# Performance work log

Hardware: AMD Instinct MI355X
Metric: run time of the kernel (lower is better)

## Reference

```python
import jax, jax.numpy as jnp
import numpy as np

SOFTCAP = 50.0
EPS = 1e-6
N_HEADS, D_HEAD = 16, 64


def _rms(x, w):
    return x * jax.lax.rsqrt(jnp.mean(x * x, axis=-1, keepdims=True) + EPS) * w


def _rope(x, cos, sin):
    # Faithful to source: apply_rope uses x.size(1) as the position axis, but is
    # called on (B, H, T, Dh) tensors, so positions are indexed by HEAD index.
    n = x.shape[1]
    x1, x2 = x[..., 0::2], x[..., 1::2]
    c = cos[:n][None, :, None, :]
    s = sin[:n][None, :, None, :]
    return jnp.stack([x1 * c - x2 * s, x1 * s + x2 * c], axis=-1).reshape(x.shape)


def setup_inputs() -> dict:
    key = jax.random.key(0)
    ks = jax.random.split(key, 12)
    L, D, H, Dh, Dff, V, B, T = 6, 1024, N_HEADS, D_HEAD, 4096, 32000, 1, 1024
    r = lambda k, shape: jax.random.normal(k, shape, dtype=jnp.float32) * 0.02
    return {
        'x': jax.random.randint(ks[0], (B, T), 0, V, dtype=jnp.int32),
        'embed': r(ks[1], (V, D)),
        'ln1': jnp.ones((L, D), jnp.float32),
        'Wq': r(ks[2], (L, H * Dh, D)),
        'Wk': r(ks[3], (L, H * Dh, D)),
        'Wv': r(ks[4], (L, H * Dh, D)),
        'Wo': r(ks[5], (L, D, H * Dh)),
        'qn': jnp.ones((L, Dh), jnp.float32),
        'kn': jnp.ones((L, Dh), jnp.float32),
        'ln2': jnp.ones((L, D), jnp.float32),
        'Wg': r(ks[6], (L, Dff, D)),
        'Wu': r(ks[7], (L, Dff, D)),
        'Wd': r(ks[8], (L, D, Dff)),
        'ln_out': jnp.ones((D,), jnp.float32),
    }


def reference(x, embed, ln1, Wq, Wk, Wv, Wo, qn, kn, ln2, Wg, Wu, Wd, ln_out):
    B, T = x.shape
    H, Dh = N_HEADS, D_HEAD
    scale = Dh ** -0.5
    # RoPE tables (theta=10000)
    freqs = 1.0 / (10000.0 ** (jnp.arange(0, Dh, 2, dtype=jnp.float32) / Dh))
    ang = jnp.arange(T, dtype=jnp.float32)[:, None] * freqs[None, :]
    cos, sin = jnp.cos(ang), jnp.sin(ang)
    mask = jnp.triu(jnp.ones((T, T), dtype=bool), k=1)  # True above diagonal

    h = embed[x]  # (B, T, D)

    def block(h, p):
        l1, wq, wk, wv, wo, qnw, knw, l2, wg, wu, wd = p
        hn = _rms(h, l1)
        q = (hn @ wq.T).reshape(B, T, H, Dh).transpose(0, 2, 1, 3)  # (B,H,T,Dh)
        k = (hn @ wk.T).reshape(B, T, H, Dh).transpose(0, 2, 1, 3)
        v = (hn @ wv.T).reshape(B, T, H, Dh).transpose(0, 2, 1, 3)
        q = _rope(_rms(q, qnw), cos, sin)
        k = _rope(_rms(k, knw), cos, sin)
        scores = jnp.einsum('bhtd,bhsd->bhts', q, k) * scale
        scores = SOFTCAP * jnp.tanh(scores / SOFTCAP)
        scores = jnp.where(mask[None, None], -jnp.inf, scores)
        attn = jax.nn.softmax(scores, axis=-1)
        o = jnp.einsum('bhts,bhsd->bhtd', attn, v)
        o = o.transpose(0, 2, 1, 3).reshape(B, T, H * Dh)
        h = h + o @ wo.T
        hn2 = _rms(h, l2)
        h = h + (jax.nn.silu(hn2 @ wg.T) * (hn2 @ wu.T)) @ wd.T
        return h, None

    h, _ = jax.lax.scan(block, h, (ln1, Wq, Wk, Wv, Wo, qn, kn, ln2, Wg, Wu, Wd))
    # tied embed/head
    logits = _rms(h, ln_out) @ embed.T  # (B, T, V)
    return logits
```

## Files before the change

### kernel.cpp

```cpp
#include <hip/hip_runtime.h>
#include <math.h>
#include <type_traits>

typedef __bf16 bf16_t;
typedef bf16_t bf16x4 __attribute__((ext_vector_type(4)));
typedef bf16_t bf16x8 __attribute__((ext_vector_type(8)));
typedef float  f32x4  __attribute__((ext_vector_type(4)));

#define RMS_EPS 1e-6f

enum { EP_STORE = 0, EP_RESID = 1, EP_SPLIT = 2, EP_SILU = 3, EP_QKV = 4 };

static __device__ __forceinline__ f32x4 mfma16(bf16x8 a, bf16x8 b, f32x4 c) {
    return __builtin_amdgcn_mfma_f32_16x16x32_bf16(a, b, c, 0, 0, 0);
}

#define GLDS(gp, lp) __builtin_amdgcn_global_load_lds( \
    (const __attribute__((address_space(1))) void*)(gp), \
    (__attribute__((address_space(3))) void*)(lp), 16, 0, 0)

template<int N> static __device__ __forceinline__ void vmwait() {
    if constexpr (N == 0)      asm volatile("s_waitcnt vmcnt(0)" ::: "memory");
    else if constexpr (N == 2) asm volatile("s_waitcnt vmcnt(2)" ::: "memory");
    else if constexpr (N == 3) asm volatile("s_waitcnt vmcnt(3)" ::: "memory");
    else if constexpr (N == 4) asm volatile("s_waitcnt vmcnt(4)" ::: "memory");
    else if constexpr (N == 6) asm volatile("s_waitcnt vmcnt(6)" ::: "memory");
    else if constexpr (N == 8) asm volatile("s_waitcnt vmcnt(8)" ::: "memory");
    __builtin_amdgcn_sched_barrier(0);
}
static __device__ __forceinline__ void bar() { __builtin_amdgcn_s_barrier(); }

template<int BM, int BN, int WR, int WC, int PLANES, int EPIL, int MINW, int DEPTH>
__global__ __launch_bounds__(WR * WC * 64, MINW)
void gemm_bf16(const bf16_t* __restrict__ Ah, const bf16_t* __restrict__ Al,
               const bf16_t* __restrict__ Bh,
               float* __restrict__ Cf, bf16_t* __restrict__ Ch, bf16_t* __restrict__ Cl,
               int K, int lda, int ldb, int ldc, long long sC,
               const float* __restrict__ qnw, const float* __restrict__ knw)
{
    constexpr int ASZ = BM * 32, BSZ = BN * 32;
    constexpr int NW = WR * WC;
    constexpr int NLD = (BM / 16 * (PLANES >= 2 ? 2 : 1) + BN / 16) / NW;
    __shared__ __align__(16) bf16_t sAh[DEPTH][ASZ], sBh[DEPTH][BSZ];
    __shared__ __align__(16) bf16_t sAl[PLANES >= 2 ? DEPTH : 1][PLANES >= 2 ? ASZ : 8];

    const int gx = gridDim.x;
    int id = blockIdx.x + gx * blockIdx.y;
    if (gridDim.z == 1) {
        int nwg = gx * gridDim.y;
        int q = nwg >> 3, r = nwg & 7;
        int xcd = id & 7, ix = id >> 3;
        id = (xcd < r ? xcd * (q + 1) : r * (q + 1) + (xcd - r) * q) + ix;
    }
    const int bm = id % gx, bn = id / gx;
    const int row0 = bm * BM, col0 = bn * BN;

    const size_t kofs = (size_t)blockIdx.z * K;
    Ah += kofs;  Bh += kofs;
    if constexpr (PLANES >= 2) Al += kofs;

    const int tid = threadIdx.x, lane = tid & 63, wave = tid >> 6;
    const int lr = lane & 15, lg = lane >> 4;
    constexpr int WM = BM / WR, WN = BN / WC, MF = WM / 16, NF = WN / 16;
    const int wr = wave / WC, wc = wave % WC;

    f32x4 acc[MF][NF];
    #pragma unroll
    for (int m = 0; m < MF; ++m)
        #pragma unroll
        for (int n = 0; n < NF; ++n) acc[m][n] = (f32x4){0.f, 0.f, 0.f, 0.f};

    auto stage = [&](int k0, int p) {
        #pragma unroll
        for (int i = wave; i < BM / 16; i += NW) {
            int s = i * 64 + lane, rr = s >> 2, c = s & 3;
            size_t go = (size_t)(row0 + rr) * lda + k0 + ((c ^ ((rr >> 1) & 3)) << 3);
            GLDS(Ah + go, &sAh[p][i * 512]);
            if constexpr (PLANES >= 2) GLDS(Al + go, &sAl[p][i * 512]);
        }
        #pragma unroll
        for (int i = wave; i < BN / 16; i += NW) {
            int s = i * 64 + lane, rr = s >> 2, c = s & 3;
            size_t go = (size_t)(col0 + rr) * ldb + k0 + ((c ^ ((rr >> 1) & 3)) << 3);
            GLDS(Bh + go, &sBh[p][i * 512]);
        }
    };

    auto compute = [&](int p) {
        bf16x8 ahf[MF], alf[MF], bhf[NF];
        #pragma unroll
        for (int m = 0; m < MF; ++m) {
            int rr = wr * WM + m * 16 + lr;
            int by = rr * 64 + ((lg ^ ((rr >> 1) & 3)) << 4);
            ahf[m] = *(const bf16x8*)((const char*)&sAh[p][0] + by);
            if constexpr (PLANES >= 2)
                alf[m] = *(const bf16x8*)((const char*)&sAl[p][0] + by);
        }
        #pragma unroll
        for (int n = 0; n < NF; ++n) {
            int rr = wc * WN + n * 16 + lr;
            int by = rr * 64 + ((lg ^ ((rr >> 1) & 3)) << 4);
            bhf[n] = *(const bf16x8*)((const char*)&sBh[p][0] + by);
        }
        #pragma unroll
        for (int m = 0; m < MF; ++m)
            #pragma unroll
            for (int n = 0; n < NF; ++n) {
                acc[m][n] = mfma16(ahf[m], bhf[n], acc[m][n]);
                if constexpr (PLANES >= 2)
                    acc[m][n] = mfma16(alf[m], bhf[n], acc[m][n]);
            }
    };

    if constexpr (DEPTH == 3) {
        const int NC = K >> 5;
        stage(0, 0);
        stage(32, 1);
        for (int j = 0; j + 2 < NC; ++j) {
            stage(32 * (j + 2), (j + 2) % 3);
            vmwait<2 * NLD>(); bar();
            compute(j % 3);
            bar();
        }
        vmwait<NLD>(); bar();
        compute((K >> 5) >= 2 ? ((K >> 5) - 2) % 3 : 0);
        vmwait<0>(); bar();
        compute(((K >> 5) - 1) % 3);
    } else {
        stage(0, 0);
        int k0 = 32;
        for (; k0 + 32 < K; k0 += 64) {
            stage(k0, 1);
            vmwait<NLD>(); bar();
            compute(0);
            bar();
            stage(k0 + 32, 0);
            vmwait<NLD>(); bar();
            compute(1);
            bar();
        }
        stage(k0, 1);
        vmwait<NLD>(); bar();
        compute(0);
        bar();
        vmwait<0>(); bar();
        compute(1);
    }

    if constexpr (EPIL == EP_QKV) {
        const int colbase = col0 + wc * WN;
        const int typ = colbase >> 10;
        const float* nw = (typ == 0) ? qnw : knw;
        const int hh = (colbase - typ * 1024) >> 6;
        constexpr float kLogF = -0.41524101186092029f;
        #pragma unroll
        for (int m = 0; m < MF; ++m)
            #pragma unroll
            for (int r = 0; r < 4; ++r) {
                int grow = row0 + wr * WM + m * 16 + lg * 4 + r;
                if (typ < 2) {
                    float ss = 0.f;
                    #pragma unroll
                    for (int n = 0; n < NF; ++n) {
                        float v = acc[m][n][r];
                        ss += v * v;
                    }
                    ss += __shfl_xor(ss, 1, 64);
                    ss += __shfl_xor(ss, 2, 64);
                    ss += __shfl_xor(ss, 4, 64);
                    ss += __shfl_xor(ss, 8, 64);
                    float inv = rsqrtf(ss * (1.0f / 64.0f) + RMS_EPS);
                    #pragma unroll
                    for (int n = 0; n < NF; ++n) {
                        int i = n * 16 + lr;
                        float x = acc[m][n][r] * inv * nw[i];
                        float p = __shfl_xor(x, 1, 64);
                        float f = exp2f((float)(i >> 1) * kLogF);
                        float ang = (float)hh * f;
                        float cs = cosf(ang), sn = sinf(ang);
                        float o = (lr & 1) ? (p * sn + x * cs) : (x * cs - p * sn);
                        Ch[(size_t)grow * ldc + colbase + i] = (bf16_t)o;
                    }
                } else {
                    #pragma unroll
                    for (int n = 0; n < NF; ++n) {
                        float v = acc[m][n][r];
                        size_t off = (size_t)grow * ldc + colbase + n * 16 + lr;
                        bf16_t hb = (bf16_t)v;
                        Ch[off] = hb;
                        Cl[off] = (bf16_t)(v - (float)hb);
                    }
                }
            }
        return;
    }

    #pragma unroll
    for (int m = 0; m < MF; ++m)
        #pragma unroll
        for (int n = 0; n < NF; ++n)
            #pragma unroll
            for (int r = 0; r < 4; ++r) {
                int grow = row0 + wr * WM + m * 16 + lg * 4 + r;
                int gcol = col0 + wc * WN + n * 16 + lr;
                float v = acc[m][n][r];
                if constexpr (EPIL == EP_SILU) {
                    float pv = __shfl_xor(v, 1, 64);
                    if (!(lr & 1)) {
                        float s = (v / (1.0f + __expf(-v))) * pv;
                        size_t off = (size_t)grow * ldc + (gcol >> 1);
                        Ch[off] = (bf16_t)s;
                    }
                } else {
                    size_t off = (size_t)blockIdx.z * sC + (size_t)grow * ldc + gcol;
                    if constexpr (EPIL == EP_STORE) {
                        Cf[off] = v;
                    } else if constexpr (EPIL == EP_RESID) {
                        Cf[off] += v;
                    } else {
                        bf16_t hb = (bf16_t)v;
                        Ch[off] = hb;
                        Cl[off] = (bf16_t)(v - (float)hb);
                    }
                }
            }
}

static __device__ __forceinline__ void wsplit_body(
    int b2, int tid,
    const float* wq, const float* wk, const float* wv, const float* wo,
    const float* wg, const float* wu, const float* wd,
    bf16_t* wAh, bf16_t* wGUh, bf16_t* wdh)
{
    #pragma unroll
    for (int k = 0; k < 4; ++k) {
        int b = b2 * 4 + k;
        const float* src;
        bf16_t* dst;
        size_t so, doff;
        if (b < 4096) {
            src = b < 1024 ? wq : b < 2048 ? wk : b < 3072 ? wv : wo;
            so = (size_t)(b & 1023) * 256 + tid;
            doff = (size_t)b * 256 + tid;
            dst = wAh;
        } else if (b < 12288) {
            int bb = b - 4096;
            int row = bb < 4096 ? 2 * bb : 2 * (bb - 4096) + 1;
            src = bb < 4096 ? wg : wu;
            so = (size_t)(bb & 4095) * 256 + tid;
            doff = (size_t)row * 256 + tid;
            dst = wGUh;
        } else {
            src = wd;
            so = (size_t)(b - 12288) * 256 + tid;
            doff = so;
            dst = wdh;
        }
        f32x4 v = ((const f32x4*)src)[so];
        bf16x4 hv;
        #pragma unroll
        for (int j = 0; j < 4; ++j) hv[j] = (bf16_t)v[j];
        ((bf16x4*)dst)[doff] = hv;
    }
}

__global__ __launch_bounds__(256)
void reduce_rms_wsplit(const float* __restrict__ p, float* __restrict__ h,
                       const float* __restrict__ w, bf16_t* __restrict__ outh,
                       const float* wq, const float* wk, const float* wv,
                       const float* wo, const float* wg, const float* wu,
                       const float* wd, bf16_t* wAh, bf16_t* wGUh, bf16_t* wdh)
{
    int blk = blockIdx.x, tid = threadIdx.x;
    if (blk >= 1024) {
        if (wq) wsplit_body(blk - 1024, tid, wq, wk, wv, wo, wg, wu, wd,
                            wAh, wGUh, wdh);
        return;
    }
    size_t i = (size_t)blk * 256 + tid;
    const size_t S = (1024 * 1024) / 4;
    f32x4 a = ((const f32x4*)p)[i];
    f32x4 b = ((const f32x4*)p)[i + S];
    f32x4 c = ((const f32x4*)p)[i + 2 * S];
    f32x4 d = ((const f32x4*)p)[i + 3 * S];
    f32x4 hv = ((const f32x4*)h)[i];
    #pragma unroll
    for (int j = 0; j < 4; ++j) hv[j] += (a[j] + b[j]) + (c[j] + d[j]);
    ((f32x4*)h)[i] = hv;

    float ss = hv[0]*hv[0] + hv[1]*hv[1] + hv[2]*hv[2] + hv[3]*hv[3];
    #pragma unroll
    for (int m = 1; m < 64; m <<= 1) ss += __shfl_xor(ss, m, 64);
    __shared__ float red[4];
    if ((tid & 63) == 0) red[tid >> 6] = ss;
    __syncthreads();
    float tot = red[0] + red[1] + red[2] + red[3];
    float inv = rsqrtf(tot * (1.0f / 1024.0f) + RMS_EPS);
    f32x4 wt4 = *(const f32x4*)(w + tid * 4);
    bf16x4 hv4;
    #pragma unroll
    for (int j = 0; j < 4; ++j) hv4[j] = (bf16_t)(hv[j] * inv * wt4[j]);
    ((bf16x4*)outh)[i] = hv4;
}

__global__ __launch_bounds__(256)
void gather_rms_wsplit(const int* __restrict__ ids, const float* __restrict__ embed,
                       const float* __restrict__ w, float* __restrict__ h,
                       bf16_t* __restrict__ outh,
                       const float* wq, const float* wk, const float* wv,
                       const float* wo, const float* wg, const float* wu,
                       const float* wd, bf16_t* wAh, bf16_t* wGUh, bf16_t* wdh)
{
    int blk = blockIdx.x, tid = threadIdx.x;
    if (blk >= 1024) {
        wsplit_body(blk - 1024, tid, wq, wk, wv, wo, wg, wu, wd, wAh, wGUh, wdh);
        return;
    }
    int row = ids[blk];
    f32x4 v = ((const f32x4*)(embed + (size_t)row * 1024))[tid];
    ((f32x4*)(h + (size_t)blk * 1024))[tid] = v;

    float ss = v[0]*v[0] + v[1]*v[1] + v[2]*v[2] + v[3]*v[3];
    #pragma unroll
    for (int m = 1; m < 64; m <<= 1) ss += __shfl_xor(ss, m, 64);
    __shared__ float red[4];
    if ((tid & 63) == 0) red[tid >> 6] = ss;
    __syncthreads();
    float tot = red[0] + red[1] + red[2] + red[3];
    float inv = rsqrtf(tot * (1.0f / 1024.0f) + RMS_EPS);
    f32x4 wt4 = *(const f32x4*)(w + tid * 4);
    bf16x4 hv;
    #pragma unroll
    for (int j = 0; j < 4; ++j) hv[j] = (bf16_t)(v[j] * inv * wt4[j]);
    ((bf16x4*)outh)[(size_t)blk * 256 + tid] = hv;
}

__global__ __launch_bounds__(128, 2)
void flash_attn(const bf16_t* __restrict__ qkvh,
                const bf16_t* __restrict__ vTh, const bf16_t* __restrict__ vTl,
                bf16_t* __restrict__ oh)
{
    __shared__ __align__(16) bf16_t sQ[32*64], sK[64*64], sVh[64*64], sVl[64*64];
    __shared__ __align__(16) bf16_t sPh[32*64], sPl[32*64];

    const int q0 = blockIdx.x * 32;
    const int hh = blockIdx.y;
    const int tid = threadIdx.x, lane = tid & 63, w = tid >> 6;
    const int lr = lane & 15, lg = lane >> 4;

    #pragma unroll
    for (int ii = 0; ii < 2; ++ii) {
        int r0 = w * 16 + ii * 8;
        int r  = r0 + (lane >> 3);
        int i  = lane & 7;
        GLDS(qkvh + (size_t)(q0 + r) * 3072 + hh * 64 + ((i ^ (r & 7)) << 3),
             sQ + r0 * 64);
    }
    __syncthreads();

    bf16x8 qa[2];
    #pragma unroll
    for (int ks = 0; ks < 2; ++ks) {
        int r = w * 16 + lr;
        qa[ks] = *(const bf16x8*)((const char*)sQ + r * 128 +
                                  ((((ks << 2) | lg) ^ (r & 7)) << 4));
    }

    f32x4 o_acc[4];
    #pragma unroll
    for (int n = 0; n < 4; ++n) o_acc[n] = (f32x4){0.f, 0.f, 0.f, 0.f};
    float m_run[4] = {-1e30f, -1e30f, -1e30f, -1e30f};
    float l_run[4] = {0.f, 0.f, 0.f, 0.f};

    const int ntiles = ((q0 + 31) >> 6) + 1;
    for (int t = 0; t < ntiles; ++t) {
        const int kv0 = t * 64;
        #pragma unroll
        for (int ii = 0; ii < 4; ++ii) {
            int r0 = w * 32 + ii * 8;
            int r  = r0 + (lane >> 3);
            int i  = lane & 7;
            GLDS(qkvh + (size_t)(kv0 + r) * 3072 + 1024 + hh * 64 + ((i ^ (r & 7)) << 3),
                 sK + r0 * 64);
            GLDS(vTh + (size_t)(hh * 64 + r) * 1024 + kv0 + ((i ^ (r & 7)) << 3),
                 sVh + r0 * 64);
            GLDS(vTl + (size_t)(hh * 64 + r) * 1024 + kv0 + ((i ^ (r & 7)) << 3),
                 sVl + r0 * 64);
        }
        __syncthreads();

        f32x4 s_acc[4];
        #pragma unroll
        for (int n = 0; n < 4; ++n) s_acc[n] = (f32x4){0.f, 0.f, 0.f, 0.f};
        #pragma unroll
        for (int ks = 0; ks < 2; ++ks)
            #pragma unroll
            for (int n = 0; n < 4; ++n) {
                int r = n * 16 + lr;
                bf16x8 kb = *(const bf16x8*)((const char*)sK + r * 128 +
                                             ((((ks << 2) | lg) ^ (r & 7)) << 4));
                s_acc[n] = mfma16(qa[ks], kb, s_acc[n]);
            }

        #pragma unroll
        for (int j = 0; j < 4; ++j) {
            int qr = q0 + w * 16 + lg * 4 + j;
            float p[4];
            float mx = -1e30f;
            #pragma unroll
            for (int n = 0; n < 4; ++n) {
                float sx = s_acc[n][j] * (0.125f * 0.02f);
                float v = 50.f * (1.f - 2.f / (1.f + __expf(2.f * sx)));
                int key = kv0 + n * 16 + lr;
                if (key > qr) v = -1e30f;
                p[n] = v;
                mx = fmaxf(mx, v);
            }
            #pragma unroll
            for (int m = 1; m < 16; m <<= 1) mx = fmaxf(mx, __shfl_xor(mx, m, 64));
            float mn = fmaxf(m_run[j], mx);
            float ef = __expf(m_run[j] - mn);
            m_run[j] = mn;
            float rs = 0.f;
            #pragma unroll
            for (int n = 0; n < 4; ++n) {
                float e = __expf(p[n] - mn);
                p[n] = e;
                rs += e;
            }
            #pragma unroll
            for (int m = 1; m < 16; m <<= 1) rs += __shfl_xor(rs, m, 64);
            l_run[j] = l_run[j] * ef + rs;
            #pragma unroll
            for (int n = 0; n < 4; ++n) o_acc[n][j] *= ef;
            int r = w * 16 + lg * 4 + j;
            #pragma unroll
            for (int n = 0; n < 4; ++n) {
                int c = n * 16 + lr;
                int byo = r * 128 + ((((c >> 3) ^ (r & 7)) << 4)) + ((c & 7) << 1);
                bf16_t hb = (bf16_t)p[n];
                *(bf16_t*)((char*)sPh + byo) = hb;
                *(bf16_t*)((char*)sPl + byo) = (bf16_t)(p[n] - (float)hb);
            }
        }

        #pragma unroll
        for (int ks = 0; ks < 2; ++ks) {
            int pr = w * 16 + lr;
            int pby = pr * 128 + ((((ks << 2) | lg) ^ (pr & 7)) << 4);
            bf16x8 pa  = *(const bf16x8*)((const char*)sPh + pby);
            bf16x8 pl_ = *(const bf16x8*)((const char*)sPl + pby);
            #pragma unroll
            for (int n = 0; n < 4; ++n) {
                int vr = n * 16 + lr;
                int vby = vr * 128 + ((((ks << 2) | lg) ^ (vr & 7)) << 4);
                bf16x8 vhf = *(const bf16x8*)((const char*)sVh + vby);
                bf16x8 vlf = *(const bf16x8*)((const char*)sVl + vby);
                o_acc[n] = mfma16(pa,  vhf, o_acc[n]);
                o_acc[n] = mfma16(pl_, vhf, o_acc[n]);
                o_acc[n] = mfma16(pa,  vlf, o_acc[n]);
            }
        }
        __syncthreads();
    }

    #pragma unroll
    for (int j = 0; j < 4; ++j) {
        float inv = 1.0f / l_run[j];
        int qr = q0 + w * 16 + lg * 4 + j;
        #pragma unroll
        for (int n = 0; n < 4; ++n) {
            size_t off = (size_t)qr * 1024 + hh * 64 + n * 16 + lr;
            oh[off] = (bf16_t)(o_acc[n][j] * inv);
        }
    }
}

__global__ __launch_bounds__(256)
void split_kernel(const float* __restrict__ src, bf16_t* __restrict__ hi)
{
    size_t i = (size_t)blockIdx.x * 256 + threadIdx.x;
    f32x4 v = ((const f32x4*)src)[i];
    bf16x4 hv;
    #pragma unroll
    for (int j = 0; j < 4; ++j) hv[j] = (bf16_t)v[j];
    ((bf16x4*)hi)[i] = hv;
}

__global__ __launch_bounds__(256)
void rmsnorm_split(const float* __restrict__ in, const float* __restrict__ w,
                   bf16_t* __restrict__ outh)
{
    int row = blockIdx.x, tid = threadIdx.x;
    f32x4 v = *(const f32x4*)(in + (size_t)row * 1024 + tid * 4);
    float ss = v[0]*v[0] + v[1]*v[1] + v[2]*v[2] + v[3]*v[3];
    #pragma unroll
    for (int m = 1; m < 64; m <<= 1) ss += __shfl_xor(ss, m, 64);
    __shared__ float red[4];
    if ((tid & 63) == 0) red[tid >> 6] = ss;
    __syncthreads();
    float tot = red[0] + red[1] + red[2] + red[3];
    float inv = rsqrtf(tot * (1.0f / 1024.0f) + RMS_EPS);
    f32x4 wt4 = *(const f32x4*)(w + tid * 4);
    bf16x4 hv;
    #pragma unroll
    for (int j = 0; j < 4; ++j) hv[j] = (bf16_t)(v[j] * inv * wt4[j]);
    ((bf16x4*)outh)[(size_t)row * 256 + tid] = hv;
}

__global__ __launch_bounds__(256)
void transpose_v(const bf16_t* __restrict__ qkvh, const bf16_t* __restrict__ qkvl,
                 bf16_t* __restrict__ vTh, bf16_t* __restrict__ vTl)
{
    __shared__ bf16_t tile[32][33];
    int b = blockIdx.x;
    int z = b >> 10, rem = b & 1023;
    const bf16_t* in = z ? qkvl : qkvh;
    bf16_t* out      = z ? vTl : vTh;
    int bx = (rem & 31) * 32, by = (rem >> 5) * 32;
    int r = threadIdx.x >> 5, c = threadIdx.x & 31;
    #pragma unroll
    for (int rr = r; rr < 32; rr += 8)
        tile[rr][c] = in[(size_t)(by + rr) * 3072 + 2048 + bx + c];
    __syncthreads();
    #pragma unroll
    for (int rr = r; rr < 32; rr += 8)
        out[(size_t)(bx + rr) * 1024 + by + c] = tile[c][rr];
}

extern "C" void kernel_launch(void* const* d_in, const int* in_sizes, int n_in,
                              void* d_out, int out_size, void* d_ws, size_t ws_size,
                              hipStream_t stream)
{
    (void)in_sizes; (void)n_in; (void)out_size; (void)ws_size;
    const int*   x_ids = (const int*)  d_in[0];
    const float* embed = (const float*)d_in[1];
    const float* ln1   = (const float*)d_in[2];
    const float* Wq    = (const float*)d_in[3];
    const float* Wk    = (const float*)d_in[4];
    const float* Wv    = (const float*)d_in[5];
    const float* Wo    = (const float*)d_in[6];
    const float* qn    = (const float*)d_in[7];
    const float* kn    = (const float*)d_in[8];
    const float* ln2   = (const float*)d_in[9];
    const float* Wg    = (const float*)d_in[10];
    const float* Wu    = (const float*)d_in[11];
    const float* Wd    = (const float*)d_in[12];
    const float* lnout = (const float*)d_in[13];
    float* out = (float*)d_out;

    char* ws = (char*)d_ws;
    const size_t MB = 1 << 20;
    float*  h    = (float*) (ws +   0 * MB);
    bf16_t* hnh  = (bf16_t*)(ws +   4 * MB);
    bf16_t* qkvh = (bf16_t*)(ws +   8 * MB);
    bf16_t* qkvl = (bf16_t*)(ws +  14 * MB);
    bf16_t* vTh  = (bf16_t*)(ws +  20 * MB);
    bf16_t* vTl  = (bf16_t*)(ws +  22 * MB);
    bf16_t* oh   = (bf16_t*)(ws +  24 * MB);
    bf16_t* wAh  = (bf16_t*)(ws +  28 * MB);
    bf16_t* wGUh = (bf16_t*)(ws +  36 * MB);
    bf16_t* wdh  = (bf16_t*)(ws +  52 * MB);
    bf16_t* silh = (bf16_t*)(ws +  60 * MB);
    float*  wdp  = (float*) (ws +  68 * MB);
    bf16_t* eh   = (bf16_t*)(ws +  84 * MB);

    const long long M1 = 1024 * 1024;

    gather_rms_wsplit<<<5120, 256, 0, stream>>>(
        x_ids, embed, ln1, h, hnh,
        Wq, Wk, Wv, Wo, Wg, Wu, Wd, wAh, wGUh, wdh);

    for (int l = 0; l < 6; ++l) {
        gemm_bf16<64,128,2,2,1,EP_QKV,4,3><<<dim3(16,24),256,0,stream>>>(
            hnh, nullptr, wAh, nullptr, qkvh, qkvl, 1024, 1024, 1024, 3072, 0,
            qn + l * 64, kn + l * 64);

        transpose_v<<<2048, 256, 0, stream>>>(qkvh, qkvl, vTh, vTl);

        flash_attn<<<dim3(32,16), 128, 0, stream>>>(qkvh, vTh, vTl, oh);

        gemm_bf16<64,64,2,2,1,EP_RESID,4,3><<<dim3(16,16),256,0,stream>>>(
            oh, nullptr, wAh + 3 * M1, h, nullptr, nullptr, 1024, 1024, 1024, 1024, 0,
            nullptr, nullptr);

        rmsnorm_split<<<1024, 256, 0, stream>>>(h, ln2 + l * 1024, hnh);

        gemm_bf16<128,256,2,4,1,EP_SILU,4,3><<<dim3(8,32),512,0,stream>>>(
            hnh, nullptr, wGUh, nullptr, silh, nullptr, 1024, 1024, 1024, 4096, 0,
            nullptr, nullptr);

        gemm_bf16<128,128,2,2,1,EP_STORE,4,3><<<dim3(8,8,4),256,0,stream>>>(
            silh, nullptr, wdh, wdp, nullptr, nullptr, 1024, 4096, 4096, 1024, M1,
            nullptr, nullptr);

        const float* wnext = (l < 5) ? (ln1 + (l + 1) * 1024) : lnout;
        if (l < 5) {
            reduce_rms_wsplit<<<5120, 256, 0, stream>>>(
                wdp, h, wnext, hnh,
                Wq + (size_t)(l+1) * M1, Wk + (size_t)(l+1) * M1,
                Wv + (size_t)(l+1) * M1, Wo + (size_t)(l+1) * M1,
                Wg + (size_t)(l+1) * 4 * M1, Wu + (size_t)(l+1) * 4 * M1,
                Wd + (size_t)(l+1) * 4 * M1, wAh, wGUh, wdh);
        } else {
            reduce_rms_wsplit<<<1024, 256, 0, stream>>>(
                wdp, h, wnext, hnh,
                nullptr, nullptr, nullptr, nullptr, nullptr, nullptr, nullptr,
                wAh, wGUh, wdh);
        }
    }

    split_kernel<<<32000, 256, 0, stream>>>(embed, eh);
    gemm_bf16<256,256,2,4,1,EP_STORE,2,2><<<dim3(4,125),512,0,stream>>>(
        hnh, nullptr, eh, out, nullptr, nullptr, 1024, 1024, 1024, 32000, 0,
        nullptr, nullptr);
}
```

Baseline: 1.176 ms.

## Add dedicated logits GEMM with split-K-chunk double buffering and XCD remap

Replaces the generic bf16 GEMM used for the final logits projection with a specialized 256x256 kernel. K is processed as 16 tiles of 64, each split into two 32-wide half-stages. Global-to-LDS loads for the next half-stage are issued before the MFMAs of the current one, with tuned vmcnt waits and setprio around the MFMA block. Workgroup IDs are remapped so consecutive tiles land on the same XCD. This aims to hide load latency in the largest GEMM, at the cost of hardcoded dimensions and more LDS usage.

```diff
diff --git a/kernel.cpp b/kernel.cpp
--- a/kernel.cpp
+++ b/kernel.cpp
@@ -10,6 +10,8 @@
 #define RMS_EPS 1e-6f
 
 enum { EP_STORE = 0, EP_RESID = 1, EP_SPLIT = 2, EP_SILU = 3, EP_QKV = 4 };
+
+template<int V> using IC = std::integral_constant<int, V>;
 
 static __device__ __forceinline__ f32x4 mfma16(bf16x8 a, bf16x8 b, f32x4 c) {
     return __builtin_amdgcn_mfma_f32_16x16x32_bf16(a, b, c, 0, 0, 0);
@@ -29,6 +31,10 @@
     __builtin_amdgcn_sched_barrier(0);
 }
 static __device__ __forceinline__ void bar() { __builtin_amdgcn_s_barrier(); }
+static __device__ __forceinline__ void lgkm0() {
+    asm volatile("s_waitcnt lgkmcnt(0)" ::: "memory");
+    __builtin_amdgcn_sched_barrier(0);
+}
 
 template<int BM, int BN, int WR, int WC, int PLANES, int EPIL, int MINW, int DEPTH>
 __global__ __launch_bounds__(WR * WC * 64, MINW)
@@ -226,6 +232,124 @@
             }
 }
 
+__global__ __launch_bounds__(512, 2)
+void gemm_logits8(const bf16_t* __restrict__ Ah, const bf16_t* __restrict__ Bh,
+                  float* __restrict__ Cf)
+{
+    constexpr int lda = 1024, ldb = 1024, ldc = 32000;
+    constexpr int NT = 16;
+    __shared__ __align__(16) bf16_t sA[2][2][256 * 32];
+    __shared__ __align__(16) bf16_t sB[2][2][256 * 32];
+
+    const int gx = gridDim.x;
+    int id = blockIdx.x + gx * blockIdx.y;
+    {
+        int nwg = gx * gridDim.y;
+        int q = nwg >> 3, r = nwg & 7;
+        int xcd = id & 7, ix = id >> 3;
+        id = (xcd < r ? xcd * (q + 1) : r * (q + 1) + (xcd - r) * q) + ix;
+    }
+    const int bm = id % gx, bn = id / gx;
+    const int row0 = bm * 256, col0 = bn * 256;
+
+    const int tid = threadIdx.x, lane = tid & 63, wave = tid >> 6;
+    const int lr = lane & 15, lg = lane >> 4;
+    const int wr = wave >> 2, wc = wave & 3;
+
+    f32x4 acc[8][4];
+    #pragma unroll
+    for (int m = 0; m < 8; ++m)
+        #pragma unroll
+        for (int n = 0; n < 4; ++n) acc[m][n] = (f32x4){0.f, 0.f, 0.f, 0.f};
+
+    auto stageA = [&](int chunk, int buf, int ks) {
+        int k0 = chunk * 32;
+        #pragma unroll
+        for (int i = wave; i < 16; i += 8) {
+            int s = i * 64 + lane, rr = s >> 2, c = s & 3;
+            size_t go = (size_t)(row0 + rr) * lda + k0 + ((c ^ ((rr >> 1) & 3)) << 3);
+            GLDS(Ah + go, &sA[buf][ks][i * 512]);
+        }
+    };
+    auto stageB = [&](int chunk, int buf, int ks) {
+        int k0 = chunk * 32;
+        #pragma unroll
+        for (int i = wave; i < 16; i += 8) {
+            int s = i * 64 + lane, rr = s >> 2, c = s & 3;
+            size_t go = (size_t)(col0 + rr) * ldb + k0 + ((c ^ ((rr >> 1) & 3)) << 3);
+            GLDS(Bh + go, &sB[buf][ks][i * 512]);
+        }
+    };
+
+    auto phase = [&](int t, auto ksc) {
+        constexpr int ks = decltype(ksc)::value;
+        const int buf = t & 1;
+        bf16x8 af[8], bf4[4];
+        #pragma unroll
+        for (int m = 0; m < 8; ++m) {
+            int rr = wr * 128 + m * 16 + lr;
+            int by = rr * 64 + ((lg ^ ((rr >> 1) & 3)) << 4);
+            af[m] = *(const bf16x8*)((const char*)&sA[buf][ks][0] + by);
+        }
+        #pragma unroll
+        for (int n = 0; n < 4; ++n) {
+            int rr = wc * 64 + n * 16 + lr;
+            int by = rr * 64 + ((lg ^ ((rr >> 1) & 3)) << 4);
+            bf4[n] = *(const bf16x8*)((const char*)&sB[buf][ks][0] + by);
+        }
+        if constexpr (ks == 0) {
+            if (t + 1 < NT) {
+                stageA(2 * (t + 1) + 1, (t + 1) & 1, 1);
+                stageB(2 * (t + 1) + 1, (t + 1) & 1, 1);
+                vmwait<8>();
+            } else {
+                vmwait<0>();
+            }
+        } else {
+            if (t + 2 < NT) {
+                stageA(2 * (t + 2), t & 1, 0);
+                stageB(2 * (t + 2), t & 1, 0);
+                vmwait<8>();
+            } else if (t + 1 < NT) {
+                vmwait<4>();
+            } else {
+                vmwait<0>();
+            }
+        }
+        bar();
+        lgkm0();
+        __builtin_amdgcn_s_setprio(1);
+        #pragma unroll
+        for (int m = 0; m < 8; ++m)
+            #pragma unroll
+            for (int n = 0; n < 4; ++n)
+                acc[m][n] = mfma16(af[m], bf4[n], acc[m][n]);
+        __builtin_amdgcn_s_setprio(0);
+        bar();
+    };
+
+    stageA(0, 0, 0); stageB(0, 0, 0);
+    stageA(1, 0, 1); stageB(1, 0, 1);
+    stageA(2, 1, 0); stageB(2, 1, 0);
+    vmwait<8>(); bar();
+
+    for (int t = 0; t < NT; ++t) {
+        phase(t, IC<0>{});
+        phase(t, IC<1>{});
+    }
+
+    #pragma unroll
+    for (int m = 0; m < 8; ++m)
+        #pragma unroll
+        for (int n = 0; n < 4; ++n)
+            #pragma unroll
+            for (int r = 0; r < 4; ++r) {
+                int grow = row0 + wr * 128 + m * 16 + lg * 4 + r;
+                int gcol = col0 + wc * 64 + n * 16 + lr;
+                Cf[(size_t)grow * ldc + gcol] = acc[m][n][r];
+            }
+}
+
 static __device__ __forceinline__ void wsplit_body(
     int b2, int tid,
     const float* wq, const float* wk, const float* wv, const float* wo,
@@ -611,7 +735,5 @@
     }
 
     split_kernel<<<32000, 256, 0, stream>>>(embed, eh);
-    gemm_bf16<256,256,2,4,1,EP_STORE,2,2><<<dim3(4,125),512,0,stream>>>(
-        hnh, nullptr, eh, out, nullptr, nullptr, 1024, 1024, 1024, 32000, 0,
-        nullptr, nullptr);
-}
+    gemm_logits8<<<dim3(4,125), 512, 0, stream>>>(hnh, eh, out);
+}
```

Result: no change. 1.166 ms (-0.9%).
